# Kernel optimization log

Hardware: AMD Instinct MI355X
Metric: run time of the kernel (lower is better)

The kernel has to match this reference:

```python
import jax, jax.numpy as jnp
import numpy as np


def setup_inputs() -> dict:
    key = jax.random.key(0)
    ks = jax.random.split(key, 10)
    N, E = 50000, 1600000
    IN, H, OUT = 32, 64, 16
    x = jax.random.normal(ks[0], (N, IN), dtype=jnp.float32)
    edge_index = jax.random.randint(ks[1], (2, E), 0, N, dtype=jnp.int64)
    edge_attr = jax.random.normal(ks[2], (E, 3), dtype=jnp.float32)
    s1 = 1.0 / np.sqrt(2 * IN + 3)
    W1 = jax.random.uniform(ks[3], (2 * IN + 3, H), jnp.float32, -s1, s1)
    b1 = jax.random.uniform(ks[4], (H,), jnp.float32, -s1, s1)
    s2 = 1.0 / np.sqrt(H)
    W2 = jax.random.uniform(ks[5], (H, H), jnp.float32, -s2, s2)
    b2 = jax.random.uniform(ks[6], (H,), jnp.float32, -s2, s2)
    Wo = jax.random.uniform(ks[7], (H, OUT), jnp.float32, -s2, s2)
    bo = jax.random.uniform(ks[8], (OUT,), jnp.float32, -s2, s2)
    return {"x": x, "edge_index": edge_index, "edge_attr": edge_attr,
            "W1": W1, "b1": b1, "W2": W2, "b2": b2, "Wo": Wo, "bo": bo}


def reference(x, edge_index, edge_attr, W1, b1, W2, b2, Wo, bo):
    N = x.shape[0]
    src, dst = edge_index[0], edge_index[1]  # PyG: x_j = x[src], x_i = x[dst]
    x_i = x[dst]                      # [E, IN]
    x_j = x[src]                      # [E, IN]
    tmp = jnp.concatenate([x_i, x_j - x_i, edge_attr], axis=1)  # [E, 2*IN+3]
    h = jax.nn.relu(tmp @ W1 + b1)    # [E, H]
    msg = h @ W2 + b2                 # [E, H]
    # max-aggregate messages to destination nodes; empty segments -> 0 (PyG fill)
    agg = jax.ops.segment_max(msg, dst, num_segments=N)
    agg = jnp.where(jnp.isfinite(agg), agg, 0.0)
    out = jax.nn.sigmoid(agg @ Wo + bo)  # [N, OUT]
    return out
```

## Files before the change

kernel.cpp:

```cpp
#include <hip/hip_runtime.h>

#define IN_F 32
#define HID 64
#define OUTF 16
#define NSUB 8
#define SB_CAP 16
#define OVF_CAP 65536
#define ORD_NEG_INF 0x007FFFFFu

typedef _Float16 v8h __attribute__((ext_vector_type(8)));
typedef float v4f __attribute__((ext_vector_type(4)));

__device__ __forceinline__ unsigned ordenc(float v) {
  unsigned b = __float_as_uint(v);
  return (b & 0x80000000u) ? ~b : (b | 0x80000000u);
}
__device__ __forceinline__ float orddec(unsigned u) {
  unsigned b = (u & 0x80000000u) ? (u & 0x7FFFFFFFu) : ~u;
  return __uint_as_float(b);
}
__device__ __forceinline__ unsigned short f2h_bits(float f) {
  _Float16 h = (_Float16)f; unsigned short u; __builtin_memcpy(&u, &h, 2); return u;
}
__device__ __forceinline__ float h_bits2f(unsigned short u) {
  _Float16 h; __builtin_memcpy(&h, &u, 2); return (float)h;
}

__global__ __launch_bounds__(256) void pre_scatter_kernel(
    const float* __restrict__ x, const int* __restrict__ ei,
    const float* __restrict__ ea, const float* __restrict__ W1,
    const float* __restrict__ b1,
    float* __restrict__ P, _Float16* __restrict__ Q,
    uint2* __restrict__ rec, int* __restrict__ cnt,
    int* __restrict__ ovf, int* __restrict__ ovf_cnt,
    int E, int N, int nSB)
{
  if (blockIdx.x < (unsigned)nSB) {
    const int t = threadIdx.x;
    const int base = blockIdx.x * 1024;
    const int g = blockIdx.x & (NSUB - 1);
    int e[4], s[4], d[4], pos[4];
    bool v[4];
#pragma unroll
    for (int i = 0; i < 4; ++i) {
      e[i] = base + i * 256 + t;
      v[i] = e[i] < E;
      int ec = v[i] ? e[i] : 0;
      s[i] = ei[ec];
      d[i] = ei[(size_t)E + ec];
    }
#pragma unroll
    for (int i = 0; i < 4; ++i)
      pos[i] = v[i] ? atomicAdd(&cnt[d[i] * NSUB + g], 1) : SB_CAP;
    float a0[4], a1[4], a2[4];
#pragma unroll
    for (int i = 0; i < 4; ++i) {
      int ec = v[i] ? e[i] : 0;
      a0[i] = ea[ec * 3 + 0]; a1[i] = ea[ec * 3 + 1]; a2[i] = ea[ec * 3 + 2];
    }
#pragma unroll
    for (int i = 0; i < 4; ++i) {
      if (!v[i]) continue;
      if (pos[i] < SB_CAP) {
        uint2 r;
        r.x = (unsigned)s[i] | ((unsigned)f2h_bits(a0[i]) << 16);
        r.y = (unsigned)f2h_bits(a1[i]) | ((unsigned)f2h_bits(a2[i]) << 16);
        rec[((size_t)d[i] * NSUB + g) * SB_CAP + pos[i]] = r;
      } else {
        int oi = atomicAdd(ovf_cnt, 1);
        if (oi < OVF_CAP) ovf[oi] = e[i];
      }
    }
    return;
  }
  const int lane = threadIdx.x & 63;
  float w1d[IN_F], w1b[IN_F];
#pragma unroll
  for (int c = 0; c < IN_F; ++c) {
    w1b[c] = W1[(IN_F + c) * HID + lane];
    w1d[c] = W1[c * HID + lane] - w1b[c];
  }
  const float b1v = b1[lane];
  int gw = __builtin_amdgcn_readfirstlane((((int)blockIdx.x - nSB) << 2) | (threadIdx.x >> 6));
  const int nwaves = 512 << 2;
  for (int n = gw; n < N; n += nwaves) {
    float p = b1v, q = 0.f;
#pragma unroll
    for (int c = 0; c < IN_F; ++c) {
      float xv = x[n * IN_F + c];
      p = fmaf(xv, w1d[c], p);
      q = fmaf(xv, w1b[c], q);
    }
    P[n * HID + lane] = p;
    Q[n * HID + lane] = (_Float16)q;
  }
}

__global__ __launch_bounds__(256) void bucket_kernel(
    const uint2* __restrict__ rec, const int* __restrict__ cnt,
    const float* __restrict__ W1, const float* __restrict__ W2,
    const float* __restrict__ P, const _Float16* __restrict__ Q,
    unsigned* __restrict__ agg, int N)
{
  __shared__ __align__(16) _Float16 hB[4][16][72];

  const int wave = threadIdx.x >> 6;
  const int lane = threadIdx.x & 63;
  const int quad = lane >> 4;
  const int eidx = lane & 15;
  const int mych = ((eidx >> 2) << 4) + (quad << 2) + (eidx & 3);

  v8h a_frag[4][2];
#pragma unroll
  for (int t = 0; t < 4; ++t)
#pragma unroll
    for (int ks = 0; ks < 2; ++ks)
#pragma unroll
      for (int j = 0; j < 8; ++j)
        a_frag[t][ks][j] = (_Float16)W2[(ks * 32 + quad * 8 + j) * HID + t * 16 + eidx];

  const float w1c0 = W1[(2 * IN_F + 0) * HID + lane];
  const float w1c1 = W1[(2 * IN_F + 1) * HID + lane];
  const float w1c2 = W1[(2 * IN_F + 2) * HID + lane];

  const int gwave = __builtin_amdgcn_readfirstlane((blockIdx.x << 2) | wave);
  const int nw = gridDim.x << 2;

  int d = gwave;
  if (d >= N) return;

  int m; uint2 r0, r1; float pP;
  auto prefetch = [&](int dd) {
    const uint4 ca = *(const uint4*)&cnt[(size_t)dd * NSUB];
    const uint4 cb = *(const uint4*)&cnt[(size_t)dd * NSUB + 4];
    int c0 = min((int)ca.x, SB_CAP), c1 = min((int)ca.y, SB_CAP);
    int c2 = min((int)ca.z, SB_CAP), c3 = min((int)ca.w, SB_CAP);
    int c4 = min((int)cb.x, SB_CAP), c5 = min((int)cb.y, SB_CAP);
    int c6 = min((int)cb.z, SB_CAP), c7 = min((int)cb.w, SB_CAP);
    int p1 = c0, p2 = p1 + c1, p3 = p2 + c2, p4 = p3 + c3;
    int p5 = p4 + c4, p6 = p5 + c5, p7 = p6 + c6;
    m = p7 + c7;
    {
      const int i = lane;
      if (i < m) {
        int g = 0, base = 0;
        if (i >= p1) { g = 1; base = p1; }
        if (i >= p2) { g = 2; base = p2; }
        if (i >= p3) { g = 3; base = p3; }
        if (i >= p4) { g = 4; base = p4; }
        if (i >= p5) { g = 5; base = p5; }
        if (i >= p6) { g = 6; base = p6; }
        if (i >= p7) { g = 7; base = p7; }
        r0 = rec[((size_t)dd * NSUB + g) * SB_CAP + (i - base)];
      }
    }
    if (m > 64) {
      const int i = 64 + lane;
      if (i < m) {
        int g = 0, base = 0;
        if (i >= p1) { g = 1; base = p1; }
        if (i >= p2) { g = 2; base = p2; }
        if (i >= p3) { g = 3; base = p3; }
        if (i >= p4) { g = 4; base = p4; }
        if (i >= p5) { g = 5; base = p5; }
        if (i >= p6) { g = 6; base = p6; }
        if (i >= p7) { g = 7; base = p7; }
        r1 = rec[((size_t)dd * NSUB + g) * SB_CAP + (i - base)];
      }
    }
    pP = P[(size_t)dd * HID + lane];
  };

  prefetch(d);

  while (d < N) {
    const int dn = d + nw;
    const int m_cur = m;
    const float pvl = pP;
    uint2 ra = r0, rb = r1;

    if (m_cur > 0) {
      {
        const int lm = m_cur - 1;
        unsigned rlx, rly;
        if (lm < 64) {
          rlx = (unsigned)__builtin_amdgcn_readlane((int)ra.x, lm);
          rly = (unsigned)__builtin_amdgcn_readlane((int)ra.y, lm);
        } else {
          rlx = (unsigned)__builtin_amdgcn_readlane((int)rb.x, lm & 63);
          rly = (unsigned)__builtin_amdgcn_readlane((int)rb.y, lm & 63);
        }
        if (lane >= m_cur)      { ra.x = rlx; ra.y = rly; }
        if (lane + 64 >= m_cur) { rb.x = rlx; rb.y = rly; }
      }

      float qv[16];
#pragma unroll
      for (int i = 0; i < 16; ++i) {
        unsigned sx = (unsigned)__builtin_amdgcn_readlane((int)ra.x, i) & 0xFFFFu;
        qv[i] = (float)Q[(size_t)sx * HID + lane];
      }

      if (dn < N) prefetch(dn);

      float maxv[4][4];
#pragma unroll
      for (int t = 0; t < 4; ++t)
#pragma unroll
        for (int r = 0; r < 4; ++r) maxv[t][r] = -INFINITY;

      const int ntile = (m_cur + 15) >> 4;
      for (int tb = 0; tb < ntile; ++tb) {
        const unsigned rsx = (tb < 4) ? ra.x : rb.x;
        const unsigned rsy = (tb < 4) ? ra.y : rb.y;
        const int b16 = (tb & 3) << 4;
#pragma unroll
        for (int i = 0; i < 16; ++i) {
          const unsigned rx = (unsigned)__builtin_amdgcn_readlane((int)rsx, b16 + i);
          const unsigned ry = (unsigned)__builtin_amdgcn_readlane((int)rsy, b16 + i);
          float pre = pvl + qv[i];
          pre = fmaf(h_bits2f((unsigned short)(rx >> 16)), w1c0, pre);
          pre = fmaf(h_bits2f((unsigned short)(ry & 0xFFFFu)), w1c1, pre);
          pre = fmaf(h_bits2f((unsigned short)(ry >> 16)), w1c2, pre);
          hB[wave][i][lane] = (_Float16)fmaxf(pre, 0.f);
        }
        __builtin_amdgcn_wave_barrier();

        const v8h bf0 = *(const v8h*)&hB[wave][eidx][quad * 8];
        const v8h bf1 = *(const v8h*)&hB[wave][eidx][32 + quad * 8];
        if (tb + 1 < ntile) {
          const unsigned rnx = (tb + 1 < 4) ? ra.x : rb.x;
          const int bn = ((tb + 1) & 3) << 4;
#pragma unroll
          for (int i = 0; i < 16; ++i) {
            unsigned sx = (unsigned)__builtin_amdgcn_readlane((int)rnx, bn + i) & 0xFFFFu;
            qv[i] = (float)Q[(size_t)sx * HID + lane];
          }
        }
#pragma unroll
        for (int t = 0; t < 4; ++t) {
          v4f acc = (v4f){0.f, 0.f, 0.f, 0.f};
          acc = __builtin_amdgcn_mfma_f32_16x16x32_f16(a_frag[t][0], bf0, acc, 0, 0, 0);
          acc = __builtin_amdgcn_mfma_f32_16x16x32_f16(a_frag[t][1], bf1, acc, 0, 0, 0);
#pragma unroll
          for (int r = 0; r < 4; ++r) maxv[t][r] = fmaxf(maxv[t][r], acc[r]);
        }
        __builtin_amdgcn_wave_barrier();
      }

#pragma unroll
      for (int t = 0; t < 4; ++t)
#pragma unroll
        for (int r = 0; r < 4; ++r) {
          float v = maxv[t][r];
          v = fmaxf(v, __shfl_xor(v, 1, 64));
          v = fmaxf(v, __shfl_xor(v, 2, 64));
          v = fmaxf(v, __shfl_xor(v, 4, 64));
          v = fmaxf(v, __shfl_xor(v, 8, 64));
          maxv[t][r] = v;
        }
      float val = maxv[0][0];
#pragma unroll
      for (int t = 0; t < 4; ++t)
#pragma unroll
        for (int r = 0; r < 4; ++r)
          val = (eidx == t * 4 + r) ? maxv[t][r] : val;
      agg[(size_t)d * HID + mych] = ordenc(val);
    } else {
      if (dn < N) prefetch(dn);
      agg[(size_t)d * HID + lane] = ORD_NEG_INF;
    }
    d = dn;
  }
}

__global__ __launch_bounds__(256) void overflow_kernel(
    const int* __restrict__ ei, const float* __restrict__ ea,
    const float* __restrict__ W1, const float* __restrict__ W2,
    const float* __restrict__ P, const _Float16* __restrict__ Q,
    const int* __restrict__ ovf, const int* __restrict__ ovf_cnt,
    unsigned* __restrict__ agg, int E)
{
  __shared__ float hsh[4][HID];
  const int wave = threadIdx.x >> 6;
  const int lane = threadIdx.x & 63;

  int M = *ovf_cnt;
  if (M > OVF_CAP) M = OVF_CAP;
  if (M == 0) return;

  float w2r[HID];
#pragma unroll
  for (int j = 0; j < HID; ++j) w2r[j] = W2[j * HID + lane];
  const float w1c0 = W1[(2 * IN_F + 0) * HID + lane];
  const float w1c1 = W1[(2 * IN_F + 1) * HID + lane];
  const float w1c2 = W1[(2 * IN_F + 2) * HID + lane];

  const int gwave = __builtin_amdgcn_readfirstlane((blockIdx.x << 2) | wave);
  const int nw = gridDim.x << 2;
  for (int k = gwave; k < M; k += nw) {
    int e = ovf[k];
    int s = ei[e];
    int d = ei[(size_t)E + e];
    float pre = P[(size_t)d * HID + lane] + (float)Q[(size_t)s * HID + lane];
    pre = fmaf(ea[e * 3 + 0], w1c0, pre);
    pre = fmaf(ea[e * 3 + 1], w1c1, pre);
    pre = fmaf(ea[e * 3 + 2], w1c2, pre);
    hsh[wave][lane] = fmaxf(pre, 0.f);
    __builtin_amdgcn_wave_barrier();
    float mv = 0.f;
#pragma unroll
    for (int j = 0; j < HID; ++j) mv = fmaf(hsh[wave][j], w2r[j], mv);
    atomicMax(&agg[(size_t)d * HID + lane], ordenc(mv));
    __builtin_amdgcn_wave_barrier();
  }
}

__global__ __launch_bounds__(256) void out_kernel(
    const unsigned* __restrict__ agg,
    const float* __restrict__ b2,
    const float* __restrict__ Wo, const float* __restrict__ bo,
    float* __restrict__ out, int N)
{
  __shared__ float Wos[HID * OUTF];
  __shared__ float bos[OUTF];
  __shared__ float b2s[HID];
  __shared__ float aggs[16][HID + 1];

  for (int i = threadIdx.x; i < HID * OUTF; i += 256) Wos[i] = Wo[i];
  if (threadIdx.x < OUTF) bos[threadIdx.x] = bo[threadIdx.x];
  if (threadIdx.x < HID) b2s[threadIdx.x] = b2[threadIdx.x];
  __syncthreads();

  const int nodeBase = blockIdx.x * 16;
  {
    int ln = threadIdx.x >> 4;
    int k0 = (threadIdx.x & 15) * 4;
    int n = nodeBase + ln;
    if (n < N) {
      const uint4 u = *(const uint4*)&agg[(size_t)n * HID + k0];
      aggs[ln][k0 + 0] = (u.x == ORD_NEG_INF) ? 0.f : orddec(u.x) + b2s[k0 + 0];
      aggs[ln][k0 + 1] = (u.y == ORD_NEG_INF) ? 0.f : orddec(u.y) + b2s[k0 + 1];
      aggs[ln][k0 + 2] = (u.z == ORD_NEG_INF) ? 0.f : orddec(u.z) + b2s[k0 + 2];
      aggs[ln][k0 + 3] = (u.w == ORD_NEG_INF) ? 0.f : orddec(u.w) + b2s[k0 + 3];
    }
  }
  __syncthreads();
  {
    int ln = threadIdx.x >> 4;
    int o = threadIdx.x & 15;
    int n = nodeBase + ln;
    if (n < N) {
      float acc = bos[o];
#pragma unroll
      for (int k = 0; k < HID; ++k) acc = fmaf(aggs[ln][k], Wos[k * OUTF + o], acc);
      out[n * OUTF + o] = 1.f / (1.f + __expf(-acc));
    }
  }
}

extern "C" void kernel_launch(void* const* d_in, const int* in_sizes, int n_in,
                              void* d_out, int out_size, void* d_ws, size_t ws_size,
                              hipStream_t stream) {
  const float* x  = (const float*)d_in[0];
  const int*   ei = (const int*)d_in[1];
  const float* ea = (const float*)d_in[2];
  const float* W1 = (const float*)d_in[3];
  const float* b1 = (const float*)d_in[4];
  const float* W2 = (const float*)d_in[5];
  const float* b2 = (const float*)d_in[6];
  const float* Wo = (const float*)d_in[7];
  const float* bo = (const float*)d_in[8];
  float* out = (float*)d_out;

  const int N = in_sizes[0] / IN_F;
  const int E = in_sizes[1] / 2;

  char* w = (char*)d_ws;
  float*     Pp  = (float*)w;                    w += (size_t)N * HID * 4;
  _Float16*  Qp  = (_Float16*)w;                 w += (size_t)N * HID * 2;
  unsigned*  agg = (unsigned*)w;                 w += (size_t)N * HID * 4;
  uint2*     rec = (uint2*)w;                    w += (size_t)N * NSUB * SB_CAP * 8;
  int*       cnt = (int*)w;                      w += (size_t)N * NSUB * 4;
  int*   ovf_cnt = (int*)w;                      w += 16;
  int*       ovf = (int*)w;

  hipMemsetAsync(cnt, 0, (size_t)N * NSUB * 4 + 16, stream);

  const int nSB = (E + 1023) / 1024;
  pre_scatter_kernel<<<nSB + 512, 256, 0, stream>>>(
      x, ei, ea, W1, b1, Pp, Qp, rec, cnt, ovf, ovf_cnt, E, N, nSB);
  bucket_kernel<<<4096, 256, 0, stream>>>(rec, cnt, W1, W2, Pp, Qp, agg, N);
  overflow_kernel<<<256, 256, 0, stream>>>(ei, ea, W1, W2, Pp, Qp, ovf, ovf_cnt, agg, E);
  out_kernel<<<(N + 15) / 16, 256, 0, stream>>>(agg, b2, Wo, bo, out, N);
}
```

Baseline: 290.0 us.

## Restructure edge pre-activation to 8-channel-per-lane vector layout with fp32 Q

Changes the bucket kernel's layer-1 pre-activation so each lane handles 8 channels for two edges, not one channel for 16 edges. Q gathers become 32-byte vector loads per lane with lane shuffles for the source indices, and each lane writes a single packed uint4 to LDS. Q is stored as fp32 instead of fp16, which removes conversions but doubles Q storage and gather bandwidth. The goal is fewer readlane/scalar ops and fewer narrow gather and LDS instructions, in exchange for more gathered bytes and shuffle overhead.

```diff
diff --git a/kernel.cpp b/kernel.cpp
--- a/kernel.cpp
+++ b/kernel.cpp
@@ -10,6 +10,7 @@
 
 typedef _Float16 v8h __attribute__((ext_vector_type(8)));
 typedef float v4f __attribute__((ext_vector_type(4)));
+typedef float v2f __attribute__((ext_vector_type(2)));
 
 __device__ __forceinline__ unsigned ordenc(float v) {
   unsigned b = __float_as_uint(v);
@@ -30,7 +31,7 @@
     const float* __restrict__ x, const int* __restrict__ ei,
     const float* __restrict__ ea, const float* __restrict__ W1,
     const float* __restrict__ b1,
-    float* __restrict__ P, _Float16* __restrict__ Q,
+    float* __restrict__ P, float* __restrict__ Q,
     uint2* __restrict__ rec, int* __restrict__ cnt,
     int* __restrict__ ovf, int* __restrict__ ovf_cnt,
     int E, int N, int nSB)
@@ -92,14 +93,14 @@
       q = fmaf(xv, w1b[c], q);
     }
     P[n * HID + lane] = p;
-    Q[n * HID + lane] = (_Float16)q;
+    Q[n * HID + lane] = q;
   }
 }
 
 __global__ __launch_bounds__(256) void bucket_kernel(
     const uint2* __restrict__ rec, const int* __restrict__ cnt,
     const float* __restrict__ W1, const float* __restrict__ W2,
-    const float* __restrict__ P, const _Float16* __restrict__ Q,
+    const float* __restrict__ P, const float* __restrict__ Q,
     unsigned* __restrict__ agg, int N)
 {
   __shared__ __align__(16) _Float16 hB[4][16][72];
@@ -109,6 +110,8 @@
   const int quad = lane >> 4;
   const int eidx = lane & 15;
   const int mych = ((eidx >> 2) << 4) + (quad << 2) + (eidx & 3);
+  const int cg  = lane & 7;
+  const int el0 = lane >> 3;
 
   v8h a_frag[4][2];
 #pragma unroll
@@ -119,9 +122,13 @@
       for (int j = 0; j < 8; ++j)
         a_frag[t][ks][j] = (_Float16)W2[(ks * 32 + quad * 8 + j) * HID + t * 16 + eidx];
 
-  const float w1c0 = W1[(2 * IN_F + 0) * HID + lane];
-  const float w1c1 = W1[(2 * IN_F + 1) * HID + lane];
-  const float w1c2 = W1[(2 * IN_F + 2) * HID + lane];
+  v2f w0v[4], w1v[4], w2v[4];
+#pragma unroll
+  for (int k = 0; k < 4; ++k) {
+    w0v[k] = *(const v2f*)&W1[(2 * IN_F + 0) * HID + cg * 8 + 2 * k];
+    w1v[k] = *(const v2f*)&W1[(2 * IN_F + 1) * HID + cg * 8 + 2 * k];
+    w2v[k] = *(const v2f*)&W1[(2 * IN_F + 2) * HID + cg * 8 + 2 * k];
+  }
 
   const int gwave = __builtin_amdgcn_readfirstlane((blockIdx.x << 2) | wave);
   const int nw = gridDim.x << 2;
@@ -129,7 +136,7 @@
   int d = gwave;
   if (d >= N) return;
 
-  int m; uint2 r0, r1; float pP;
+  int m; uint2 r0, r1; v2f pvN[4];
   auto prefetch = [&](int dd) {
     const uint4 ca = *(const uint4*)&cnt[(size_t)dd * NSUB];
     const uint4 cb = *(const uint4*)&cnt[(size_t)dd * NSUB + 4];
@@ -168,7 +175,9 @@
         r1 = rec[((size_t)dd * NSUB + g) * SB_CAP + (i - base)];
       }
     }
-    pP = P[(size_t)dd * HID + lane];
+#pragma unroll
+    for (int k = 0; k < 4; ++k)
+      pvN[k] = *(const v2f*)&P[(size_t)dd * HID + cg * 8 + 2 * k];
   };
 
   prefetch(d);
@@ -176,8 +185,10 @@
   while (d < N) {
     const int dn = d + nw;
     const int m_cur = m;
-    const float pvl = pP;
     uint2 ra = r0, rb = r1;
+    v2f pv[4];
+#pragma unroll
+    for (int k = 0; k < 4; ++k) pv[k] = pvN[k];
 
     if (m_cur > 0) {
       {
@@ -194,11 +205,14 @@
         if (lane + 64 >= m_cur) { rb.x = rlx; rb.y = rly; }
       }
 
-      float qv[16];
-#pragma unroll
-      for (int i = 0; i < 16; ++i) {
-        unsigned sx = (unsigned)__builtin_amdgcn_readlane((int)ra.x, i) & 0xFFFFu;
-        qv[i] = (float)Q[(size_t)sx * HID + lane];
+      v2f qA[4], qB[4];
+      {
+        unsigned sx0 = (unsigned)__shfl((int)ra.x, el0, 64) & 0xFFFFu;
+        unsigned sx1 = (unsigned)__shfl((int)ra.x, el0 + 8, 64) & 0xFFFFu;
+        const v2f* q0 = (const v2f*)&Q[(size_t)sx0 * HID + cg * 8];
+        const v2f* q1 = (const v2f*)&Q[(size_t)sx1 * HID + cg * 8];
+#pragma unroll
+        for (int k = 0; k < 4; ++k) { qA[k] = q0[k]; qB[k] = q1[k]; }
       }
 
       if (dn < N) prefetch(dn);
@@ -214,29 +228,61 @@
         const unsigned rsx = (tb < 4) ? ra.x : rb.x;
         const unsigned rsy = (tb < 4) ? ra.y : rb.y;
         const int b16 = (tb & 3) << 4;
-#pragma unroll
-        for (int i = 0; i < 16; ++i) {
-          const unsigned rx = (unsigned)__builtin_amdgcn_readlane((int)rsx, b16 + i);
-          const unsigned ry = (unsigned)__builtin_amdgcn_readlane((int)rsy, b16 + i);
-          float pre = pvl + qv[i];
-          pre = fmaf(h_bits2f((unsigned short)(rx >> 16)), w1c0, pre);
-          pre = fmaf(h_bits2f((unsigned short)(ry & 0xFFFFu)), w1c1, pre);
-          pre = fmaf(h_bits2f((unsigned short)(ry >> 16)), w1c2, pre);
-          hB[wave][i][lane] = (_Float16)fmaxf(pre, 0.f);
-        }
-        __builtin_amdgcn_wave_barrier();
-
-        const v8h bf0 = *(const v8h*)&hB[wave][eidx][quad * 8];
-        const v8h bf1 = *(const v8h*)&hB[wave][eidx][32 + quad * 8];
+
+        const unsigned rx0 = (unsigned)__shfl((int)rsx, b16 + el0, 64);
+        const unsigned ry0 = (unsigned)__shfl((int)rsy, b16 + el0, 64);
+        const unsigned rx1 = (unsigned)__shfl((int)rsx, b16 + el0 + 8, 64);
+        const unsigned ry1 = (unsigned)__shfl((int)rsy, b16 + el0 + 8, 64);
+        const float a00 = h_bits2f((unsigned short)(rx0 >> 16));
+        const float a01 = h_bits2f((unsigned short)(ry0 & 0xFFFFu));
+        const float a02 = h_bits2f((unsigned short)(ry0 >> 16));
+        const float a10 = h_bits2f((unsigned short)(rx1 >> 16));
+        const float a11 = h_bits2f((unsigned short)(ry1 & 0xFFFFu));
+        const float a12 = h_bits2f((unsigned short)(ry1 >> 16));
+
+        v2f pA[4], pB[4];
+#pragma unroll
+        for (int k = 0; k < 4; ++k) { pA[k] = pv[k] + qA[k]; pB[k] = pv[k] + qB[k]; }
+#pragma unroll
+        for (int k = 0; k < 4; ++k) { pA[k] += a00 * w0v[k]; pB[k] += a10 * w0v[k]; }
+#pragma unroll
+        for (int k = 0; k < 4; ++k) { pA[k] += a01 * w1v[k]; pB[k] += a11 * w1v[k]; }
+#pragma unroll
+        for (int k = 0; k < 4; ++k) { pA[k] += a02 * w2v[k]; pB[k] += a12 * w2v[k]; }
+
         if (tb + 1 < ntile) {
           const unsigned rnx = (tb + 1 < 4) ? ra.x : rb.x;
           const int bn = ((tb + 1) & 3) << 4;
-#pragma unroll
-          for (int i = 0; i < 16; ++i) {
-            unsigned sx = (unsigned)__builtin_amdgcn_readlane((int)rnx, bn + i) & 0xFFFFu;
-            qv[i] = (float)Q[(size_t)sx * HID + lane];
+          unsigned sx0 = (unsigned)__shfl((int)rnx, bn + el0, 64) & 0xFFFFu;
+          unsigned sx1 = (unsigned)__shfl((int)rnx, bn + el0 + 8, 64) & 0xFFFFu;
+          const v2f* q0 = (const v2f*)&Q[(size_t)sx0 * HID + cg * 8];
+          const v2f* q1 = (const v2f*)&Q[(size_t)sx1 * HID + cg * 8];
+#pragma unroll
+          for (int k = 0; k < 4; ++k) { qA[k] = q0[k]; qB[k] = q1[k]; }
+        }
+
+        {
+          uint4 u;
+          unsigned hw[4];
+#pragma unroll
+          for (int k = 0; k < 4; ++k) {
+            float x0 = fmaxf(pA[k].x, 0.f), x1 = fmaxf(pA[k].y, 0.f);
+            hw[k] = (unsigned)f2h_bits(x0) | ((unsigned)f2h_bits(x1) << 16);
           }
+          u.x = hw[0]; u.y = hw[1]; u.z = hw[2]; u.w = hw[3];
+          *(uint4*)&hB[wave][el0][cg * 8] = u;
+#pragma unroll
+          for (int k = 0; k < 4; ++k) {
+            float x0 = fmaxf(pB[k].x, 0.f), x1 = fmaxf(pB[k].y, 0.f);
+            hw[k] = (unsigned)f2h_bits(x0) | ((unsigned)f2h_bits(x1) << 16);
+          }
+          u.x = hw[0]; u.y = hw[1]; u.z = hw[2]; u.w = hw[3];
+          *(uint4*)&hB[wave][el0 + 8][cg * 8] = u;
         }
+        __builtin_amdgcn_wave_barrier();
+
+        const v8h bf0 = *(const v8h*)&hB[wave][eidx][quad * 8];
+        const v8h bf1 = *(const v8h*)&hB[wave][eidx][32 + quad * 8];
 #pragma unroll
         for (int t = 0; t < 4; ++t) {
           v4f acc = (v4f){0.f, 0.f, 0.f, 0.f};
@@ -277,7 +323,7 @@
 __global__ __launch_bounds__(256) void overflow_kernel(
     const int* __restrict__ ei, const float* __restrict__ ea,
     const float* __restrict__ W1, const float* __restrict__ W2,
-    const float* __restrict__ P, const _Float16* __restrict__ Q,
+    const float* __restrict__ P, const float* __restrict__ Q,
     const int* __restrict__ ovf, const int* __restrict__ ovf_cnt,
     unsigned* __restrict__ agg, int E)
 {
@@ -302,7 +348,7 @@
     int e = ovf[k];
     int s = ei[e];
     int d = ei[(size_t)E + e];
-    float pre = P[(size_t)d * HID + lane] + (float)Q[(size_t)s * HID + lane];
+    float pre = P[(size_t)d * HID + lane] + Q[(size_t)s * HID + lane];
     pre = fmaf(ea[e * 3 + 0], w1c0, pre);
     pre = fmaf(ea[e * 3 + 1], w1c1, pre);
     pre = fmaf(ea[e * 3 + 2], w1c2, pre);
@@ -378,7 +424,7 @@
 
   char* w = (char*)d_ws;
   float*     Pp  = (float*)w;                    w += (size_t)N * HID * 4;
-  _Float16*  Qp  = (_Float16*)w;                 w += (size_t)N * HID * 2;
+  float*     Qp  = (float*)w;                    w += (size_t)N * HID * 4;
   unsigned*  agg = (unsigned*)w;                 w += (size_t)N * HID * 4;
   uint2*     rec = (uint2*)w;                    w += (size_t)N * NSUB * SB_CAP * 8;
   int*       cnt = (int*)w;                      w += (size_t)N * NSUB * 4;
```

New measurement: 312.4 us. +7.7%, slower.

## Replace atomic per-node sub-bucket scatter with two-pass counting sort by destination

Applied to the files above, without the earlier changes.

Replaces the single-pass scatter, which did a global atomicAdd per edge into 8 sub-buckets per node, with a counting sort. A per-block histogram over 128-node buckets is followed by a scan, a coarse scatter into bucket arrays, and a per-bucket LDS pass that writes contiguous per-node record slots. This removes contended global atomics and the prefix-sum gather logic in the bucket kernel's prefetch, so each node's records become one contiguous read. The cost is two extra kernel launches and extra intermediate traffic for the coarse buckets. Overflow records now carry fp16 edge attributes and the destination directly.

```diff
diff --git a/kernel.cpp b/kernel.cpp
--- a/kernel.cpp
+++ b/kernel.cpp
@@ -3,8 +3,9 @@
 #define IN_F 32
 #define HID 64
 #define OUTF 16
-#define NSUB 8
-#define SB_CAP 16
+#define DPB 128
+#define CAPB 5120
+#define RSL 80
 #define OVF_CAP 65536
 #define ORD_NEG_INF 0x007FFFFFu
 
@@ -26,51 +27,31 @@
   _Float16 h; __builtin_memcpy(&h, &u, 2); return (float)h;
 }
 
-__global__ __launch_bounds__(256) void pre_scatter_kernel(
-    const float* __restrict__ x, const int* __restrict__ ei,
-    const float* __restrict__ ea, const float* __restrict__ W1,
+__global__ __launch_bounds__(256) void p0_kernel(
+    const int* __restrict__ ei,
+    const float* __restrict__ x, const float* __restrict__ W1,
     const float* __restrict__ b1,
     float* __restrict__ P, _Float16* __restrict__ Q,
-    uint2* __restrict__ rec, int* __restrict__ cnt,
-    int* __restrict__ ovf, int* __restrict__ ovf_cnt,
-    int E, int N, int nSB)
+    unsigned* __restrict__ hist, int E, int N, int nSB, int NBKT)
 {
   if (blockIdx.x < (unsigned)nSB) {
-    const int t = threadIdx.x;
+    __shared__ unsigned h[512];
+    for (int i = threadIdx.x; i < NBKT; i += 256) h[i] = 0;
+    __syncthreads();
     const int base = blockIdx.x * 1024;
-    const int g = blockIdx.x & (NSUB - 1);
-    int e[4], s[4], d[4], pos[4];
-    bool v[4];
+    int d[4]; bool v[4];
 #pragma unroll
     for (int i = 0; i < 4; ++i) {
-      e[i] = base + i * 256 + t;
-      v[i] = e[i] < E;
-      int ec = v[i] ? e[i] : 0;
-      s[i] = ei[ec];
-      d[i] = ei[(size_t)E + ec];
+      int e = base + i * 256 + threadIdx.x;
+      v[i] = e < E;
+      d[i] = ei[(size_t)E + (v[i] ? e : 0)];
     }
 #pragma unroll
     for (int i = 0; i < 4; ++i)
-      pos[i] = v[i] ? atomicAdd(&cnt[d[i] * NSUB + g], 1) : SB_CAP;
-    float a0[4], a1[4], a2[4];
-#pragma unroll
-    for (int i = 0; i < 4; ++i) {
-      int ec = v[i] ? e[i] : 0;
-      a0[i] = ea[ec * 3 + 0]; a1[i] = ea[ec * 3 + 1]; a2[i] = ea[ec * 3 + 2];
-    }
-#pragma unroll
-    for (int i = 0; i < 4; ++i) {
-      if (!v[i]) continue;
-      if (pos[i] < SB_CAP) {
-        uint2 r;
-        r.x = (unsigned)s[i] | ((unsigned)f2h_bits(a0[i]) << 16);
-        r.y = (unsigned)f2h_bits(a1[i]) | ((unsigned)f2h_bits(a2[i]) << 16);
-        rec[((size_t)d[i] * NSUB + g) * SB_CAP + pos[i]] = r;
-      } else {
-        int oi = atomicAdd(ovf_cnt, 1);
-        if (oi < OVF_CAP) ovf[oi] = e[i];
-      }
-    }
+      if (v[i]) atomicAdd(&h[d[i] >> 7], 1u);
+    __syncthreads();
+    for (int i = threadIdx.x; i < NBKT; i += 256)
+      hist[(size_t)blockIdx.x * NBKT + i] = h[i];
     return;
   }
   const int lane = threadIdx.x & 63;
@@ -96,6 +77,111 @@
   }
 }
 
+__global__ __launch_bounds__(256) void scan_kernel(
+    unsigned* __restrict__ hist, unsigned* __restrict__ totals,
+    int nblk, int NBKT)
+{
+  __shared__ unsigned s[256];
+  const int b = blockIdx.x;
+  const int tid = threadIdx.x;
+  unsigned running = 0;
+  const int nch = (nblk + 255) >> 8;
+  for (int c = 0; c < nch; ++c) {
+    const int idx = c * 256 + tid;
+    unsigned v = (idx < nblk) ? hist[(size_t)idx * NBKT + b] : 0u;
+    s[tid] = v;
+    __syncthreads();
+#pragma unroll
+    for (int off = 1; off < 256; off <<= 1) {
+      unsigned t = (tid >= off) ? s[tid - off] : 0u;
+      __syncthreads();
+      s[tid] += t;
+      __syncthreads();
+    }
+    const unsigned incl = s[tid];
+    const unsigned tot = s[255];
+    if (idx < nblk) hist[(size_t)idx * NBKT + b] = running + (incl - v);
+    running += tot;
+    __syncthreads();
+  }
+  if (tid == 0) totals[b] = running;
+}
+
+__global__ __launch_bounds__(256) void p1_kernel(
+    const int* __restrict__ ei, const float* __restrict__ ea,
+    const unsigned* __restrict__ hist,
+    uint2* __restrict__ cu, unsigned char* __restrict__ cdlo,
+    uint4* __restrict__ ovf, int* __restrict__ ovf_cnt,
+    int E, int NBKT)
+{
+  __shared__ unsigned h2[512];
+  for (int i = threadIdx.x; i < NBKT; i += 256) h2[i] = 0;
+  __syncthreads();
+  const int base = blockIdx.x * 1024;
+  int s[4], d[4]; bool v[4];
+#pragma unroll
+  for (int i = 0; i < 4; ++i) {
+    int e = base + i * 256 + threadIdx.x;
+    v[i] = e < E;
+    int ec = v[i] ? e : 0;
+    s[i] = ei[ec];
+    d[i] = ei[(size_t)E + ec];
+  }
+  float a0[4], a1[4], a2[4];
+#pragma unroll
+  for (int i = 0; i < 4; ++i) {
+    int ec = v[i] ? (base + i * 256 + threadIdx.x) : 0;
+    a0[i] = ea[ec * 3 + 0]; a1[i] = ea[ec * 3 + 1]; a2[i] = ea[ec * 3 + 2];
+  }
+#pragma unroll
+  for (int i = 0; i < 4; ++i) {
+    if (!v[i]) continue;
+    const int b = d[i] >> 7;
+    const unsigned r = atomicAdd(&h2[b], 1u);
+    const unsigned pos = hist[(size_t)blockIdx.x * NBKT + b] + r;
+    uint2 pay;
+    pay.x = (unsigned)s[i] | ((unsigned)f2h_bits(a0[i]) << 16);
+    pay.y = (unsigned)f2h_bits(a1[i]) | ((unsigned)f2h_bits(a2[i]) << 16);
+    if (pos < CAPB) {
+      cu[(size_t)b * CAPB + pos] = pay;
+      cdlo[(size_t)b * CAPB + pos] = (unsigned char)(d[i] & (DPB - 1));
+    } else {
+      int oi = atomicAdd(ovf_cnt, 1);
+      if (oi < OVF_CAP) ovf[oi] = make_uint4(pay.x, pay.y, (unsigned)d[i], 0u);
+    }
+  }
+}
+
+__global__ __launch_bounds__(512) void p2_kernel(
+    const uint2* __restrict__ cu, const unsigned char* __restrict__ cdlo,
+    const unsigned* __restrict__ totals,
+    uint2* __restrict__ rec, int* __restrict__ cnt,
+    uint4* __restrict__ ovf, int* __restrict__ ovf_cnt, int N)
+{
+  __shared__ int c[DPB];
+  const int b = blockIdx.x;
+  const int tid = threadIdx.x;
+  if (tid < DPB) c[tid] = 0;
+  __syncthreads();
+  const int nE = (int)min(totals[b], (unsigned)CAPB);
+  for (int i = tid; i < nE; i += 512) {
+    const uint2 pay = cu[(size_t)b * CAPB + i];
+    const int dlo = cdlo[(size_t)b * CAPB + i];
+    const int r = atomicAdd(&c[dlo], 1);
+    const int d = b * DPB + dlo;
+    if (r < RSL) rec[(size_t)d * RSL + r] = pay;
+    else {
+      int oi = atomicAdd(ovf_cnt, 1);
+      if (oi < OVF_CAP) ovf[oi] = make_uint4(pay.x, pay.y, (unsigned)d, 0u);
+    }
+  }
+  __syncthreads();
+  if (tid < DPB) {
+    const int d = b * DPB + tid;
+    if (d < N) cnt[d] = c[tid];
+  }
+}
+
 __global__ __launch_bounds__(256) void bucket_kernel(
     const uint2* __restrict__ rec, const int* __restrict__ cnt,
     const float* __restrict__ W1, const float* __restrict__ W2,
@@ -131,42 +217,10 @@
 
   int m; uint2 r0, r1; float pP;
   auto prefetch = [&](int dd) {
-    const uint4 ca = *(const uint4*)&cnt[(size_t)dd * NSUB];
-    const uint4 cb = *(const uint4*)&cnt[(size_t)dd * NSUB + 4];
-    int c0 = min((int)ca.x, SB_CAP), c1 = min((int)ca.y, SB_CAP);
-    int c2 = min((int)ca.z, SB_CAP), c3 = min((int)ca.w, SB_CAP);
-    int c4 = min((int)cb.x, SB_CAP), c5 = min((int)cb.y, SB_CAP);
-    int c6 = min((int)cb.z, SB_CAP), c7 = min((int)cb.w, SB_CAP);
-    int p1 = c0, p2 = p1 + c1, p3 = p2 + c2, p4 = p3 + c3;
-    int p5 = p4 + c4, p6 = p5 + c5, p7 = p6 + c6;
-    m = p7 + c7;
-    {
-      const int i = lane;
-      if (i < m) {
-        int g = 0, base = 0;
-        if (i >= p1) { g = 1; base = p1; }
-        if (i >= p2) { g = 2; base = p2; }
-        if (i >= p3) { g = 3; base = p3; }
-        if (i >= p4) { g = 4; base = p4; }
-        if (i >= p5) { g = 5; base = p5; }
-        if (i >= p6) { g = 6; base = p6; }
-        if (i >= p7) { g = 7; base = p7; }
-        r0 = rec[((size_t)dd * NSUB + g) * SB_CAP + (i - base)];
-      }
-    }
+    m = min(cnt[dd], RSL);
+    if (lane < m) r0 = rec[(size_t)dd * RSL + lane];
     if (m > 64) {
-      const int i = 64 + lane;
-      if (i < m) {
-        int g = 0, base = 0;
-        if (i >= p1) { g = 1; base = p1; }
-        if (i >= p2) { g = 2; base = p2; }
-        if (i >= p3) { g = 3; base = p3; }
-        if (i >= p4) { g = 4; base = p4; }
-        if (i >= p5) { g = 5; base = p5; }
-        if (i >= p6) { g = 6; base = p6; }
-        if (i >= p7) { g = 7; base = p7; }
-        r1 = rec[((size_t)dd * NSUB + g) * SB_CAP + (i - base)];
-      }
+      if (64 + lane < m) r1 = rec[(size_t)dd * RSL + 64 + lane];
     }
     pP = P[(size_t)dd * HID + lane];
   };
@@ -275,11 +329,10 @@
 }
 
 __global__ __launch_bounds__(256) void overflow_kernel(
-    const int* __restrict__ ei, const float* __restrict__ ea,
+    const uint4* __restrict__ ovf, const int* __restrict__ ovf_cnt,
     const float* __restrict__ W1, const float* __restrict__ W2,
     const float* __restrict__ P, const _Float16* __restrict__ Q,
-    const int* __restrict__ ovf, const int* __restrict__ ovf_cnt,
-    unsigned* __restrict__ agg, int E)
+    unsigned* __restrict__ agg)
 {
   __shared__ float hsh[4][HID];
   const int wave = threadIdx.x >> 6;
@@ -299,13 +352,13 @@
   const int gwave = __builtin_amdgcn_readfirstlane((blockIdx.x << 2) | wave);
   const int nw = gridDim.x << 2;
   for (int k = gwave; k < M; k += nw) {
-    int e = ovf[k];
-    int s = ei[e];
-    int d = ei[(size_t)E + e];
+    const uint4 o = ovf[k];
+    const int s = (int)(o.x & 0xFFFFu);
+    const int d = (int)o.z;
     float pre = P[(size_t)d * HID + lane] + (float)Q[(size_t)s * HID + lane];
-    pre = fmaf(ea[e * 3 + 0], w1c0, pre);
-    pre = fmaf(ea[e * 3 + 1], w1c1, pre);
-    pre = fmaf(ea[e * 3 + 2], w1c2, pre);
+    pre = fmaf(h_bits2f((unsigned short)(o.x >> 16)), w1c0, pre);
+    pre = fmaf(h_bits2f((unsigned short)(o.y & 0xFFFFu)), w1c1, pre);
+    pre = fmaf(h_bits2f((unsigned short)(o.y >> 16)), w1c2, pre);
     hsh[wave][lane] = fmaxf(pre, 0.f);
     __builtin_amdgcn_wave_barrier();
     float mv = 0.f;
@@ -375,22 +428,30 @@
 
   const int N = in_sizes[0] / IN_F;
   const int E = in_sizes[1] / 2;
+  const int NBKT = (N + DPB - 1) / DPB;
+  const int nSB  = (E + 1023) / 1024;
 
   char* w = (char*)d_ws;
-  float*     Pp  = (float*)w;                    w += (size_t)N * HID * 4;
-  _Float16*  Qp  = (_Float16*)w;                 w += (size_t)N * HID * 2;
-  unsigned*  agg = (unsigned*)w;                 w += (size_t)N * HID * 4;
-  uint2*     rec = (uint2*)w;                    w += (size_t)N * NSUB * SB_CAP * 8;
-  int*       cnt = (int*)w;                      w += (size_t)N * NSUB * 4;
-  int*   ovf_cnt = (int*)w;                      w += 16;
-  int*       ovf = (int*)w;
-
-  hipMemsetAsync(cnt, 0, (size_t)N * NSUB * 4 + 16, stream);
-
-  const int nSB = (E + 1023) / 1024;
-  pre_scatter_kernel<<<nSB + 512, 256, 0, stream>>>(
-      x, ei, ea, W1, b1, Pp, Qp, rec, cnt, ovf, ovf_cnt, E, N, nSB);
+  auto align16 = [](size_t v) { return (v + 15) & ~(size_t)15; };
+  float*     Pp   = (float*)w;       w += align16((size_t)N * HID * 4);
+  _Float16*  Qp   = (_Float16*)w;    w += align16((size_t)N * HID * 2);
+  unsigned*  agg  = (unsigned*)w;    w += align16((size_t)N * HID * 4);
+  uint2*     rec  = (uint2*)w;       w += align16((size_t)N * RSL * 8);
+  uint2*     cu   = (uint2*)w;       w += align16((size_t)NBKT * CAPB * 8);
+  unsigned*  hist = (unsigned*)w;    w += align16((size_t)nSB * NBKT * 4);
+  unsigned*  tot  = (unsigned*)w;    w += align16((size_t)NBKT * 4);
+  int*       cnt  = (int*)w;         w += align16((size_t)N * 4);
+  unsigned char* cdlo = (unsigned char*)w; w += align16((size_t)NBKT * CAPB);
+  int*   ovf_cnt  = (int*)w;         w += 16;
+  uint4*     ovf  = (uint4*)w;
+
+  hipMemsetAsync(ovf_cnt, 0, 16, stream);
+
+  p0_kernel<<<nSB + 512, 256, 0, stream>>>(ei, x, W1, b1, Pp, Qp, hist, E, N, nSB, NBKT);
+  scan_kernel<<<NBKT, 256, 0, stream>>>(hist, tot, nSB, NBKT);
+  p1_kernel<<<nSB, 256, 0, stream>>>(ei, ea, hist, cu, cdlo, ovf, ovf_cnt, E, NBKT);
+  p2_kernel<<<NBKT, 512, 0, stream>>>(cu, cdlo, tot, rec, cnt, ovf, ovf_cnt, N);
   bucket_kernel<<<4096, 256, 0, stream>>>(rec, cnt, W1, W2, Pp, Qp, agg, N);
-  overflow_kernel<<<256, 256, 0, stream>>>(ei, ea, W1, W2, Pp, Qp, ovf, ovf_cnt, agg, E);
+  overflow_kernel<<<256, 256, 0, stream>>>(ovf, ovf_cnt, W1, W2, Pp, Qp, agg);
   out_kernel<<<(N + 15) / 16, 256, 0, stream>>>(agg, b2, Wo, bo, out, N);
 }
```

Result: faster. 264.5 us (-8.8%).
